# Kernel tuning notes

Measured on AMD Instinct MI355X. Metric: run time of the kernel, lower is better.

Reference implementation:

```python
import jax, jax.numpy as jnp
import numpy as np

# V:N:M sparsity config (n=2 kept of m=8 per vector-block; mask pattern [1,0,1,0,0,0,0,0])
M_BLK = 8
KEEP_OFFSETS = np.array([0, 2], dtype=np.int32)  # positions kept in each m-block
B, S, D_IN, D_OUT = 2, 8192, 4096, 4096
K_KEPT = D_IN // M_BLK * len(KEEP_OFFSETS)  # 1024


def _keep_idx():
    # column indices of the surviving weight entries (same for every output row)
    blocks = np.arange(D_IN // M_BLK, dtype=np.int32)[:, None] * M_BLK  # [D_IN/M,1]
    return jnp.asarray((blocks + KEEP_OFFSETS[None, :]).reshape(-1))   # [K_KEPT]


def setup_inputs() -> dict:
    key = jax.random.key(0)
    k1, k2, k3 = jax.random.split(key, 3)
    x = jax.random.normal(k1, (B, S, D_IN), dtype=jnp.float32)
    values = jax.random.normal(k2, (D_OUT, K_KEPT), dtype=jnp.float32) * 0.02
    bias = jax.random.normal(k3, (D_OUT,), dtype=jnp.float32) * 0.02
    return {"x": x, "values": values, "bias": bias}


def reference(x, values, bias):
    # Sparse SpMM: gather kept input features, dense GEMM with compressed values.
    # Equivalent to x @ (masked dense W).T + bias, without materializing W.
    keep = _keep_idx()               # [K_KEPT] int32, constant metadata
    xg = x[..., keep]                # [B,S,K_KEPT]
    out = jnp.einsum('bsk,nk->bsn', xg, values) + bias  # [B,S,D_OUT]
    return out
```

## Files before the change

### kernel.cpp

```cpp
#include <hip/hip_runtime.h>
#include <hip/hip_bf16.h>


#define M_TOTAL 16384
#define DIN     4096
#define KDIM    1024
#define NDIM    4096
#define BM      128
#define BN      128
#define BKT     64

typedef unsigned short u16;
typedef unsigned int   u32;
typedef __bf16 bf16x8 __attribute__((ext_vector_type(8)));
typedef float  f32x4  __attribute__((ext_vector_type(4)));

typedef const void __attribute__((address_space(1)))* gp_t;
typedef void __attribute__((address_space(3)))*       lp_t;

__device__ __forceinline__ u16 f2bf(float f) {
    u32 u = __float_as_uint(f);
    u += 0x7FFFu + ((u >> 16) & 1u);
    return (u16)(u >> 16);
}

__global__ void compact_x_kernel(const float* __restrict__ x,
                                 u32* __restrict__ xg, int nblk) {
    int i = blockIdx.x * blockDim.x + threadIdx.x;
    const int stride = gridDim.x * blockDim.x;
    for (; i < nblk; i += stride) {
        float4 v = *reinterpret_cast<const float4*>(x + (size_t)i * 8);
        xg[i] = (u32)f2bf(v.x) | ((u32)f2bf(v.z) << 16);
    }
}

__global__ void conv_vals_kernel(const float* __restrict__ v,
                                 uint2* __restrict__ vb, int n4) {
    int i = blockIdx.x * blockDim.x + threadIdx.x;
    const int stride = gridDim.x * blockDim.x;
    for (; i < n4; i += stride) {
        float4 f = *reinterpret_cast<const float4*>(v + (size_t)i * 4);
        uint2 o;
        o.x = (u32)f2bf(f.x) | ((u32)f2bf(f.y) << 16);
        o.y = (u32)f2bf(f.z) | ((u32)f2bf(f.w) << 16);
        vb[i] = o;
    }
}

__global__ __launch_bounds__(256, 2) void gemm_kernel(
    const u16* __restrict__ A, const u16* __restrict__ Bv,
    const float* __restrict__ bias, float* __restrict__ C)
{
    __shared__ u16 As[BM * BKT];
    __shared__ u16 Bs[BN * BKT];

    const int tid  = threadIdx.x;
    const int lane = tid & 63;
    const int wid  = tid >> 6;
    const int wr   = wid >> 1;
    const int wc   = wid & 1;

    const int nbn = NDIM / BN;
    const int btm = blockIdx.x / nbn;
    const int btn = blockIdx.x % nbn;

    const int sr = tid >> 3;
    const int sc = (tid & 7) * 8;
    const size_t a_base = (size_t)(btm * BM + sr) * KDIM + sc;
    const size_t b_base = (size_t)(btn * BN + sr) * KDIM + sc;

    const int lrow = lane & 15;
    const int lko  = (lane >> 4) * 8;

    f32x4 acc[4][4] = {};

    for (int k0 = 0; k0 < KDIM; k0 += BKT) {
#pragma unroll
        for (int it = 0; it < 4; ++it) {
            __builtin_amdgcn_global_load_lds(
                (gp_t)(A + a_base + (size_t)it * 32 * KDIM + k0),
                (lp_t)(&As[it * 2048 + tid * 8]), 16, 0, 0);
            __builtin_amdgcn_global_load_lds(
                (gp_t)(Bv + b_base + (size_t)it * 32 * KDIM + k0),
                (lp_t)(&Bs[it * 2048 + tid * 8]), 16, 0, 0);
        }
        __syncthreads();

#pragma unroll
        for (int kk = 0; kk < BKT; kk += 32) {
            bf16x8 af[4], bfr[4];
#pragma unroll
            for (int m = 0; m < 4; ++m)
                af[m] = *reinterpret_cast<const bf16x8*>(
                    &As[(wr * 64 + m * 16 + lrow) * BKT + kk + lko]);
#pragma unroll
            for (int n = 0; n < 4; ++n)
                bfr[n] = *reinterpret_cast<const bf16x8*>(
                    &Bs[(wc * 64 + n * 16 + lrow) * BKT + kk + lko]);
#pragma unroll
            for (int m = 0; m < 4; ++m)
#pragma unroll
                for (int n = 0; n < 4; ++n)
                    acc[m][n] = __builtin_amdgcn_mfma_f32_16x16x32_bf16(
                        af[m], bfr[n], acc[m][n], 0, 0, 0);
        }
        __syncthreads();
    }

    const int row_base = btm * BM + wr * 64 + (lane >> 4) * 4;
    const int col_base = btn * BN + wc * 64 + lrow;
#pragma unroll
    for (int n = 0; n < 4; ++n) {
        const int col = col_base + n * 16;
        const float bv = bias[col];
#pragma unroll
        for (int m = 0; m < 4; ++m) {
            const int row = row_base + m * 16;
            f32x4 a = acc[m][n];
#pragma unroll
            for (int j = 0; j < 4; ++j)
                C[(size_t)(row + j) * NDIM + col] = a[j] + bv;
        }
    }
}

extern "C" void kernel_launch(void* const* d_in, const int* in_sizes, int n_in,
                              void* d_out, int out_size, void* d_ws, size_t ws_size,
                              hipStream_t stream) {
    const float* x      = (const float*)d_in[0];
    const float* values = (const float*)d_in[1];
    const float* bias   = (const float*)d_in[2];
    float* out = (float*)d_out;

    u16* xg = (u16*)d_ws;
    u16* vb = (u16*)((char*)d_ws + ((size_t)32 << 20));

    const int nblk = M_TOTAL * (DIN / 8);
    compact_x_kernel<<<2048, 256, 0, stream>>>(x, (u32*)xg, nblk);

    const int n4 = NDIM * KDIM / 4;
    conv_vals_kernel<<<1024, 256, 0, stream>>>(values, (uint2*)vb, n4);

    const int grid = (M_TOTAL / BM) * (NDIM / BN);
    gemm_kernel<<<grid, 256, 0, stream>>>(xg, vb, bias, out);
}
```

Measured before the change: 241.9 us.

## Rewrite GEMM as 256x256 tile, 8-wave, double-buffered LDS pipeline with swizzles

Replaces the 128x128 single-buffered GEMM with a 256x256 tile computed by 512 threads. It uses a 128KB double-buffered LDS pipeline that issues async global-to-LDS loads several stages ahead and waits with explicit vmcnt counts. It adds an XOR swizzle on the LDS layout to avoid bank conflicts, a block-index swizzle for L2 locality, and s_setprio around the MFMA bursts. The goal is to overlap memory with compute and raise data reuse, at the cost of a 128KB LDS footprint, many barriers, and hand-tuned wait counts that are easy to get wrong.

Result: no change. 245.4 us (+1.5%).

```diff
diff --git a/kernel.cpp b/kernel.cpp
--- a/kernel.cpp
+++ b/kernel.cpp
@@ -6,9 +6,6 @@
 #define DIN     4096
 #define KDIM    1024
 #define NDIM    4096
-#define BM      128
-#define BN      128
-#define BKT     64
 
 typedef unsigned short u16;
 typedef unsigned int   u32;
@@ -47,79 +44,113 @@
     }
 }
 
-__global__ __launch_bounds__(256, 2) void gemm_kernel(
+
+#define LDSA(d, kh) (((d) * 2 + (kh)) * 16384)
+#define LDSB(d, kh) (65536 + ((d) * 2 + (kh)) * 16384)
+
+#define LOADA(d, kh, mh) { _Pragma("unroll") \
+    for (int m_ = 0; m_ < 4; ++m_) \
+        af[m_] = *(const bf16x8*)(lds + LDSA(d, kh) + (wr * 8 + (mh) * 4 + m_) * 1024 + fl_off); }
+
+#define LOADB(d, kh) { _Pragma("unroll") \
+    for (int n_ = 0; n_ < 4; ++n_) \
+        bfr[n_] = *(const bf16x8*)(lds + LDSB(d, kh) + (wc * 4 + n_) * 1024 + fl_off); }
+
+#define MFMA16(mh) { \
+    __builtin_amdgcn_s_setprio(1); \
+    _Pragma("unroll") for (int m_ = 0; m_ < 4; ++m_) \
+    _Pragma("unroll") for (int n_ = 0; n_ < 4; ++n_) \
+        acc[(mh) * 4 + m_][n_] = __builtin_amdgcn_mfma_f32_16x16x32_bf16( \
+            af[m_], bfr[n_], acc[(mh) * 4 + m_][n_], 0, 0, 0); \
+    __builtin_amdgcn_s_setprio(0); }
+
+#define BAR() __builtin_amdgcn_s_barrier()
+#define VMCNT6() asm volatile("s_waitcnt vmcnt(6)" ::: "memory")
+#define VMCNT0() asm volatile("s_waitcnt vmcnt(0)" ::: "memory")
+
+__global__ __launch_bounds__(512, 2) void gemm_kernel(
     const u16* __restrict__ A, const u16* __restrict__ Bv,
     const float* __restrict__ bias, float* __restrict__ C)
 {
-    __shared__ u16 As[BM * BKT];
-    __shared__ u16 Bs[BN * BKT];
+    __shared__ __align__(1024) char lds[131072];
 
     const int tid  = threadIdx.x;
     const int lane = tid & 63;
     const int wid  = tid >> 6;
-    const int wr   = wid >> 1;
-    const int wc   = wid & 1;
+    const int wr   = wid >> 2;
+    const int wc   = wid & 3;
+    const int lrow = lane & 15;
+    const int lg   = lane >> 4;
 
-    const int nbn = NDIM / BN;
-    const int btm = blockIdx.x / nbn;
-    const int btn = blockIdx.x % nbn;
+    const int b   = blockIdx.x;
+    const int swz = (b & 7) * 128 + (b >> 3);
+    const int btm = swz >> 4;
+    const int btn = swz & 15;
 
-    const int sr = tid >> 3;
-    const int sc = (tid & 7) * 8;
-    const size_t a_base = (size_t)(btm * BM + sr) * KDIM + sc;
-    const size_t b_base = (size_t)(btn * BN + sr) * KDIM + sc;
+    const int st_r0 = wid * 16 + (lane >> 2);
+    const int st_ck = ((lane & 3) * 8) ^ ((lane & 32) >> 1);
+    const u16* Asrc = A  + (size_t)(btm * 256 + st_r0) * KDIM + st_ck;
+    const u16* Bsrc = Bv + (size_t)(btn * 256 + st_r0) * KDIM + st_ck;
+    const int dst0 = tid * 16;
 
-    const int lrow = lane & 15;
-    const int lko  = (lane >> 4) * 8;
+    const int fl_off = lrow * 64 + ((lg * 16) ^ (((lrow >> 3) & 1) << 5));
 
-    f32x4 acc[4][4] = {};
+    auto STAGE = [&](int s) {
+        const int kt = s >> 2, j = s & 3;
+        const int d = kt & 1, kh = (j >> 1) & 1;
+        const int ko = kt * 64 + kh * 32;
+        const u16* src = (j & 1) ? Bsrc : Asrc;
+        const int base = ((j & 1) ? 65536 : 0) + (d * 2 + kh) * 16384;
+        __builtin_amdgcn_global_load_lds((gp_t)(src + ko),
+            (lp_t)(lds + base + dst0), 16, 0, 0);
+        __builtin_amdgcn_global_load_lds((gp_t)(src + 128 * KDIM + ko),
+            (lp_t)(lds + base + 8192 + dst0), 16, 0, 0);
+    };
 
-    for (int k0 = 0; k0 < KDIM; k0 += BKT) {
+    f32x4 acc[8][4] = {};
+    bf16x8 af[4], bfr[4];
+
+    STAGE(0); STAGE(1); STAGE(2); STAGE(3); STAGE(4); STAGE(5); STAGE(6);
+    VMCNT6();
+    BAR();
+
+#pragma unroll 1
+    for (int t = 0; t < 7; ++t) {
+        const int s0 = 8 * t + 7;
+        LOADB(0, 0); LOADA(0, 0, 0); STAGE(s0);     BAR(); MFMA16(0); BAR();
+        LOADA(0, 0, 1);              STAGE(s0 + 1); BAR(); MFMA16(1); BAR();
+        LOADB(0, 1); LOADA(0, 1, 0); STAGE(s0 + 2); BAR(); MFMA16(0); BAR();
+        LOADA(0, 1, 1);              STAGE(s0 + 3); BAR(); MFMA16(1);
+        VMCNT6(); BAR();
+        LOADB(1, 0); LOADA(1, 0, 0); STAGE(s0 + 4); BAR(); MFMA16(0); BAR();
+        LOADA(1, 0, 1);              STAGE(s0 + 5); BAR(); MFMA16(1); BAR();
+        LOADB(1, 1); LOADA(1, 1, 0); STAGE(s0 + 6); BAR(); MFMA16(0); BAR();
+        LOADA(1, 1, 1);              STAGE(s0 + 7); BAR(); MFMA16(1);
+        VMCNT6(); BAR();
+    }
+    LOADB(0, 0); LOADA(0, 0, 0); STAGE(63);         BAR(); MFMA16(0); BAR();
+    LOADA(0, 0, 1);                                 BAR(); MFMA16(1); BAR();
+    LOADB(0, 1); LOADA(0, 1, 0);                    BAR(); MFMA16(0); BAR();
+    LOADA(0, 1, 1);                                 BAR(); MFMA16(1);
+    VMCNT0(); BAR();
+    LOADB(1, 0); LOADA(1, 0, 0);                    BAR(); MFMA16(0); BAR();
+    LOADA(1, 0, 1);                                 BAR(); MFMA16(1); BAR();
+    LOADB(1, 1); LOADA(1, 1, 0);                    BAR(); MFMA16(0); BAR();
+    LOADA(1, 1, 1);                                 BAR(); MFMA16(1);
+
+    const int c_row0 = btm * 256 + wr * 128 + lg * 4;
+    const int c_col0 = btn * 256 + wc * 64 + lrow;
+    float bv[4];
 #pragma unroll
-        for (int it = 0; it < 4; ++it) {
-            __builtin_amdgcn_global_load_lds(
-                (gp_t)(A + a_base + (size_t)it * 32 * KDIM + k0),
-                (lp_t)(&As[it * 2048 + tid * 8]), 16, 0, 0);
-            __builtin_amdgcn_global_load_lds(
-                (gp_t)(Bv + b_base + (size_t)it * 32 * KDIM + k0),
-                (lp_t)(&Bs[it * 2048 + tid * 8]), 16, 0, 0);
-        }
-        __syncthreads();
-
+    for (int n = 0; n < 4; ++n) bv[n] = bias[c_col0 + n * 16];
 #pragma unroll
-        for (int kk = 0; kk < BKT; kk += 32) {
-            bf16x8 af[4], bfr[4];
+    for (int mi = 0; mi < 8; ++mi) {
+        const int row = c_row0 + (mi >> 2) * 64 + (mi & 3) * 16;
 #pragma unroll
-            for (int m = 0; m < 4; ++m)
-                af[m] = *reinterpret_cast<const bf16x8*>(
-                    &As[(wr * 64 + m * 16 + lrow) * BKT + kk + lko]);
-#pragma unroll
-            for (int n = 0; n < 4; ++n)
-                bfr[n] = *reinterpret_cast<const bf16x8*>(
-                    &Bs[(wc * 64 + n * 16 + lrow) * BKT + kk + lko]);
-#pragma unroll
-            for (int m = 0; m < 4; ++m)
-#pragma unroll
-                for (int n = 0; n < 4; ++n)
-                    acc[m][n] = __builtin_amdgcn_mfma_f32_16x16x32_bf16(
-                        af[m], bfr[n], acc[m][n], 0, 0, 0);
-        }
-        __syncthreads();
-    }
-
-    const int row_base = btm * BM + wr * 64 + (lane >> 4) * 4;
-    const int col_base = btn * BN + wc * 64 + lrow;
-#pragma unroll
-    for (int n = 0; n < 4; ++n) {
-        const int col = col_base + n * 16;
-        const float bv = bias[col];
-#pragma unroll
-        for (int m = 0; m < 4; ++m) {
-            const int row = row_base + m * 16;
-            f32x4 a = acc[m][n];
+        for (int n = 0; n < 4; ++n) {
 #pragma unroll
             for (int j = 0; j < 4; ++j)
-                C[(size_t)(row + j) * NDIM + col] = a[j] + bv;
+                C[(size_t)(row + j) * NDIM + c_col0 + n * 16] = acc[mi][n][j] + bv[n];
         }
     }
 }
@@ -141,6 +172,6 @@
     const int n4 = NDIM * KDIM / 4;
     conv_vals_kernel<<<1024, 256, 0, stream>>>(values, (uint2*)vb, n4);
 
-    const int grid = (M_TOTAL / BM) * (NDIM / BN);
-    gemm_kernel<<<grid, 256, 0, stream>>>(xg, vb, bias, out);
+    const int grid = (M_TOTAL / 256) * (NDIM / 256);
+    gemm_kernel<<<grid, 512, 0, stream>>>(xg, vb, bias, out);
 }
```
